# Optimization experiments

Hardware: AMD Instinct MI355X
Metric: run time of the kernel (lower is better)

## Reference

```python
import jax, jax.numpy as jnp
import numpy as np

EPS = 1e-5  # BatchNorm eps (eval mode, running mean 0 / var 1)
NEG_SLOPE = 0.2


def _knn_idx(x, k):
    # x: [B,C,N] -> idx [B,N,k] (indices of k largest of negative sq dist = k nearest)
    inner = jnp.einsum('bcn,bcm->bnm', x, x)
    xx = jnp.sum(x * x, axis=1)  # [B,N]
    pd = 2.0 * inner - xx[:, :, None] - xx[:, None, :]
    return jax.lax.top_k(pd, k)[1]


def _edge_feature(x, k):
    # x: [B,C,N] -> edge features [B,2C,N,k] = concat(neighbor - center, center)
    idx = _knn_idx(x, k)                        # [B,N,k]
    xt = jnp.transpose(x, (0, 2, 1))            # [B,N,C]
    nbr = jax.vmap(lambda f, i: f[i])(xt, idx)  # [B,N,k,C] gather per batch
    ctr = jnp.broadcast_to(xt[:, :, None, :], nbr.shape)
    feat = jnp.concatenate([nbr - ctr, ctr], axis=-1)  # [B,N,k,2C]
    return jnp.transpose(feat, (0, 3, 1, 2))


def _bn(x, g, b):
    # eval-mode BatchNorm: running_mean=0, running_var=1 -> x * g/sqrt(1+eps) + b
    inv = 1.0 / np.sqrt(1.0 + EPS)
    sh = (1, -1) + (1,) * (x.ndim - 2)
    return x * (g * inv).reshape(sh) + b.reshape(sh)


def _lrelu(x):
    return jnp.where(x >= 0, x, NEG_SLOPE * x)


def _conv2d(x, w, b):  # 1x1 Conv2d: x [B,Ci,N,K], w [Ci,Co]
    return jnp.einsum('bcnk,co->bonk', x, w) + b[None, :, None, None]


def _conv1d(x, w, b):  # 1x1 Conv1d: x [B,Ci,N], w [Ci,Co]
    return jnp.einsum('bcn,co->bon', x, w) + b[None, :, None]


def setup_inputs() -> dict:
    key = jax.random.key(0)
    ks = jax.random.split(key, 24)
    B, N = 8, 4096
    rn = lambda k, sh, s=0.1: (jax.random.normal(k, sh, dtype=jnp.float32) * s)
    inp = {
        'point': jax.random.normal(ks[0], (B, 3, N), dtype=jnp.float32),
        # conv1_1: Conv2d(6,64)
        'w11': rn(ks[1], (6, 64)), 'b11': rn(ks[2], (64,)),
        'g11': jnp.ones((64,), jnp.float32), 'bb11': jnp.zeros((64,), jnp.float32),
        # conv1_2: Conv2d(6,64)
        'w12': rn(ks[3], (6, 64)), 'b12': rn(ks[4], (64,)),
        'g12': jnp.ones((64,), jnp.float32), 'bb12': jnp.zeros((64,), jnp.float32),
        # conv1_3: Conv1d(128,64)
        'w13': rn(ks[5], (128, 64)), 'b13': rn(ks[6], (64,)),
        'g13': jnp.ones((64,), jnp.float32), 'bb13': jnp.zeros((64,), jnp.float32),
        # conv1_5: Conv2d(128,64)
        'w15': rn(ks[7], (128, 64)), 'b15': rn(ks[8], (64,)),
        'g15': jnp.ones((64,), jnp.float32), 'bb15': jnp.zeros((64,), jnp.float32),
        # conv1_4: Conv1d(64,128)
        'w14': rn(ks[9], (64, 128)), 'b14': rn(ks[10], (128,)),
        'g14': jnp.ones((128,), jnp.float32), 'bb14': jnp.zeros((128,), jnp.float32),
        # fc1: Linear(128,64) + ReLU + Linear(64,3)
        'wf1': rn(ks[11], (128, 64)), 'bf1': rn(ks[12], (64,)),
        'wf2': rn(ks[13], (64, 3)), 'bf2': rn(ks[14], (3,)),
    }
    return inp


def reference(point, w11, b11, g11, bb11, w12, b12, g12, bb12,
              w13, b13, g13, bb13, w15, b15, g15, bb15,
              w14, b14, g14, bb14, wf1, bf1, wf2, bf2):
    # point: [B,3,N]
    f = _edge_feature(point, 8)                    # [B,6,N,8]
    f1 = _lrelu(_bn(_conv2d(f, w11, b11), g11, bb11)).max(axis=-1)   # [B,64,N]
    f = _edge_feature(point, 16)                   # [B,6,N,16]
    f2 = _lrelu(_bn(_conv2d(f, w12, b12), g12, bb12)).max(axis=-1)   # [B,64,N]
    f = jnp.concatenate([f1, f2], axis=1)          # [B,128,N]
    f = _lrelu(_bn(_conv1d(f, w13, b13), g13, bb13))                 # [B,64,N]
    g = _edge_feature(f, 16)                       # [B,128,N,16]
    g = _lrelu(_bn(_conv2d(g, w15, b15), g15, bb15)).max(axis=-1)    # [B,64,N]
    g = _lrelu(_bn(_conv1d(g, w14, b14), g14, bb14))                 # [B,128,N]
    feat = jnp.transpose(g, (0, 2, 1))             # [B,N,128]
    h = jax.nn.relu(feat @ wf1 + bf1) @ wf2 + bf2  # [B,N,3]
    refinepoint = h + jnp.transpose(point, (0, 2, 1))
    return feat, refinepoint
```

## Files before the change

kernel.cpp:

```cpp
#include <hip/hip_runtime.h>
#include <math.h>

#define NB 8
#define NP 4096
#define FEAT_SZ (NB * NP * 128)
#define INVBN 0.9999950000374999f
#define SPLIT 2
#define CHUNKS 32

typedef unsigned long long u64;
typedef unsigned int u32;

__device__ __forceinline__ u32 fmap(float f) {
    u32 b = __float_as_uint(f);
    return b ^ ((u32)((int)b >> 31) | 0x80000000u);
}

__device__ __forceinline__ u64 umax64(u64 a, u64 b) { return a > b ? a : b; }

__device__ __forceinline__ void kins(u64 (&v)[16], u64 key) {
    if (key <= v[15]) return;
    bool bb[16];
#pragma unroll
    for (int j = 0; j < 16; ++j) bb[j] = key > v[j];
#pragma unroll
    for (int j = 15; j >= 1; --j) v[j] = bb[j] ? (bb[j - 1] ? v[j - 1] : key) : v[j];
    if (bb[0]) v[0] = key;
}

__device__ __forceinline__ void bufpush(u64 (&v)[16], u64 &q0, u64 &q1, u64 &q2, u64 &q3,
                                        int &cnt, u64 key) {
    if (cnt < 4) {
        q0 = cnt == 0 ? key : q0;
        q1 = cnt == 1 ? key : q1;
        q2 = cnt == 2 ? key : q2;
        q3 = cnt == 3 ? key : q3;
        ++cnt;
    } else {
        kins(v, key);
    }
}

__device__ __forceinline__ void bufflush(u64 (&v)[16], u64 &q0, u64 &q1, u64 &q2, u64 &q3,
                                         int &cnt) {
    kins(v, q0); kins(v, q1); kins(v, q2); kins(v, q3);
    q0 = 0; q1 = 0; q2 = 0; q3 = 0; cnt = 0;
}

__device__ __forceinline__ void bclean(u64 (&v)[16]) {
#pragma unroll
    for (int d = 8; d; d >>= 1) {
#pragma unroll
        for (int i = 0; i < 16; ++i) {
            if ((i & d) == 0) {
                u64 a = v[i], b = v[i | d];
                bool s = a < b;
                v[i] = s ? b : a;
                v[i | d] = s ? a : b;
            }
        }
    }
}

__device__ __forceinline__ void merge_shfl(u64 (&v)[16], int off) {
    u64 o[16];
#pragma unroll
    for (int j = 0; j < 16; ++j) o[j] = __shfl_down(v[j], off);
#pragma unroll
    for (int j = 0; j < 16; ++j) {
        u64 b = o[15 - j];
        v[j] = v[j] > b ? v[j] : b;
    }
    bclean(v);
}

__device__ __forceinline__ u64 rowmax8(u64 x) {
    x = umax64(x, __shfl_xor(x, 1));
    x = umax64(x, __shfl_xor(x, 2));
    x = umax64(x, __shfl_xor(x, 4));
    return x;
}

__global__ __launch_bounds__(256) void knn_point_kernel(const float* __restrict__ point,
                                                        int* __restrict__ idxP) {
    __shared__ float4 pts[NP];
    int bt = blockIdx.x >> 7;
    int n0 = (blockIdx.x & 127) << 5;
    const float* pb = point + (size_t)bt * 3 * NP;
    for (int m = threadIdx.x; m < NP; m += 256) {
        float x = pb[m], y = pb[NP + m], z = pb[2 * NP + m];
        pts[m] = make_float4(x, y, z, fmaf(z, z, fmaf(y, y, x * x)));
    }
    __syncthreads();
    int t = threadIdx.x;
    int q = t & 7;
    float4 c = pts[n0 + (t >> 3)];
    u64 v[16];
#pragma unroll
    for (int j = 0; j < 16; ++j) v[j] = 0;
    u64 b0 = 0, b1 = 0, b2 = 0, b3 = 0;
    int cnt = 0;
    u64 th = 0;
#pragma unroll 1
    for (int o = 0; o < 8; ++o) {
#pragma unroll 4
        for (int ii = 0; ii < 64; ++ii) {
            int m = (((o << 6) + ii) << 3) + q;
            float4 p = pts[m];
            float inner = fmaf(c.z, p.z, fmaf(c.y, p.y, c.x * p.x));
            float pd = fmaf(2.0f, inner, -c.w) - p.w;
            u64 key = ((u64)fmap(pd) << 32) | (u64)(u32)~m;
            if (key > th) bufpush(v, b0, b1, b2, b3, cnt, key);
        }
        if (__any(cnt >= 3)) {
            bufflush(v, b0, b1, b2, b3, cnt);
            th = rowmax8(v[15]);
        }
    }
    bufflush(v, b0, b1, b2, b3, cnt);
    merge_shfl(v, 4);
    merge_shfl(v, 2);
    merge_shfl(v, 1);
    if (q == 0) {
        int* op = idxP + ((size_t)bt * NP + n0 + (t >> 3)) * 16;
#pragma unroll
        for (int j = 0; j < 16; ++j) op[j] = (int)~(u32)v[j];
    }
}

__global__ __launch_bounds__(256) void edge12_kernel(
    const float* __restrict__ point, const int* __restrict__ idxP,
    const float* __restrict__ w11, const float* __restrict__ b11,
    const float* __restrict__ g11, const float* __restrict__ bb11,
    const float* __restrict__ w12, const float* __restrict__ b12,
    const float* __restrict__ g12, const float* __restrict__ bb12,
    float* __restrict__ f12) {
    int lane = threadIdx.x & 63;
    int pt = blockIdx.x * 4 + (threadIdx.x >> 6);
    int bt = pt >> 12, n = pt & (NP - 1);
    const float* pb = point + (size_t)bt * 3 * NP;
    float wd1[3], wc1[3], wd2[3], wc2[3];
#pragma unroll
    for (int c = 0; c < 3; ++c) {
        wd1[c] = w11[c * 64 + lane]; wc1[c] = w11[(3 + c) * 64 + lane];
        wd2[c] = w12[c * 64 + lane]; wc2[c] = w12[(3 + c) * 64 + lane];
    }
    float s1 = g11[lane] * INVBN, sh1 = bb11[lane];
    float s2 = g12[lane] * INVBN, sh2 = bb12[lane];
    float cx = pb[n], cy = pb[NP + n], cz = pb[2 * NP + n];
    float base1 = fmaf(wc1[2], cz, fmaf(wc1[1], cy, fmaf(wc1[0], cx, b11[lane])));
    float base2 = fmaf(wc2[2], cz, fmaf(wc2[1], cy, fmaf(wc2[0], cx, b12[lane])));
    float a1 = -INFINITY, a2 = -INFINITY;
    const int* nb = idxP + (size_t)pt * 16;
#pragma unroll
    for (int j = 0; j < 16; ++j) {
        int m = nb[j];
        float ex = pb[m] - cx, ey = pb[NP + m] - cy, ez = pb[2 * NP + m] - cz;
        float y2 = fmaf(wd2[2], ez, fmaf(wd2[1], ey, fmaf(wd2[0], ex, base2)));
        float z2 = fmaf(y2, s2, sh2);
        z2 = z2 >= 0.f ? z2 : 0.2f * z2;
        a2 = fmaxf(a2, z2);
        if (j < 8) {
            float y1 = fmaf(wd1[2], ez, fmaf(wd1[1], ey, fmaf(wd1[0], ex, base1)));
            float z1 = fmaf(y1, s1, sh1);
            z1 = z1 >= 0.f ? z1 : 0.2f * z1;
            a1 = fmaxf(a1, z1);
        }
    }
    f12[((size_t)pt << 7) + lane] = a1;
    f12[((size_t)pt << 7) + 64 + lane] = a2;
}

template<int K, int O, int MODE, bool XX>
__global__ __launch_bounds__(256) void gemm_act_kernel(
        const float* __restrict__ in, const float* __restrict__ W,
        const float* __restrict__ b, const float* __restrict__ g,
        const float* __restrict__ s, float* __restrict__ outp,
        float* __restrict__ xxo) {
    __shared__ __align__(16) char smem[64 * (K + 1) * 4 + K * O * 4];
    float* A  = (float*)smem;
    float* Wl = (float*)(smem + 64 * (K + 1) * 4);
    float* Hs = (float*)smem;
    constexpr int F4R = K / 4;
#pragma unroll
    for (int i = 0; i < 64 * F4R / 256; ++i) {
        int f = threadIdx.x + i * 256;
        int pt = f / F4R, c4 = f % F4R;
        float4 v = *(const float4*)(in + ((size_t)blockIdx.x * 64 + pt) * K + c4 * 4);
        float* d = A + pt * (K + 1) + c4 * 4;
        d[0] = v.x; d[1] = v.y; d[2] = v.z; d[3] = v.w;
    }
    if constexpr (MODE == 0) {
#pragma unroll
        for (int i = 0; i < 8; ++i) {
            int f = threadIdx.x + i * 256;
            int half = f >= 1024;
            int fr = f & 1023;
            int c = fr >> 4, o4 = fr & 15;
            const float* src = half ? (W + (64 + c) * 64 + o4 * 4) : (W + c * 64 + o4 * 4);
            float4 v = *(const float4*)src;
            float* d = Wl + c * 128 + half * 64 + o4 * 4;
            d[0] = v.x; d[1] = v.y; d[2] = v.z; d[3] = v.w;
        }
    } else {
#pragma unroll
        for (int i = 0; i < K * O / 1024; ++i) {
            int f = threadIdx.x + i * 256;
            *(float4*)(Wl + f * 4) = *(const float4*)(W + f * 4);
        }
    }
    __syncthreads();
    constexpr int NO = O / 8;
    int po = threadIdx.x & 7, pp = threadIdx.x >> 3;
    int pt0 = pp * 2, o0 = po * NO;
    float acc[2][NO];
#pragma unroll
    for (int i = 0; i < NO; ++i) {
        int o = o0 + i;
        float init;
        if constexpr (MODE == 0) init = (o < 64) ? 0.f : b[o - 64];
        else init = b[o];
        acc[0][i] = init;
        acc[1][i] = init;
    }
#pragma unroll 8
    for (int kk = 0; kk < K; ++kk) {
        float a0 = A[pt0 * (K + 1) + kk];
        float a1 = A[(pt0 + 1) * (K + 1) + kk];
        float w[NO];
#pragma unroll
        for (int i4 = 0; i4 < NO / 4; ++i4) {
            float4 wv = *(const float4*)(Wl + kk * O + o0 + i4 * 4);
            w[i4 * 4 + 0] = wv.x; w[i4 * 4 + 1] = wv.y;
            w[i4 * 4 + 2] = wv.z; w[i4 * 4 + 3] = wv.w;
        }
#pragma unroll
        for (int i = 0; i < NO; ++i) {
            acc[0][i] = fmaf(a0, w[i], acc[0][i]);
            acc[1][i] = fmaf(a1, w[i], acc[1][i]);
        }
    }
    float tact[2][NO];
#pragma unroll
    for (int p = 0; p < 2; ++p) {
#pragma unroll
        for (int i = 0; i < NO; ++i) {
            int o = o0 + i;
            float a = acc[p][i];
            if constexpr (MODE == 0) {
                tact[p][i] = a;
            } else {
                float vv = fmaf(a, g[o] * INVBN, s[o]);
                tact[p][i] = vv >= 0.f ? vv : 0.2f * vv;
            }
        }
    }
#pragma unroll
    for (int p = 0; p < 2; ++p) {
        size_t rowg = (size_t)blockIdx.x * 64 + pt0 + p;
#pragma unroll
        for (int i4 = 0; i4 < NO / 4; ++i4) {
            float4 ov;
            ov.x = tact[p][i4 * 4 + 0]; ov.y = tact[p][i4 * 4 + 1];
            ov.z = tact[p][i4 * 4 + 2]; ov.w = tact[p][i4 * 4 + 3];
            *(float4*)(outp + rowg * O + o0 + i4 * 4) = ov;
        }
    }
    if constexpr (XX) {
        __syncthreads();
#pragma unroll
        for (int p = 0; p < 2; ++p)
#pragma unroll
            for (int i = 0; i < NO; ++i)
                Hs[(pt0 + p) * 65 + o0 + i] = tact[p][i];
        __syncthreads();
        if (threadIdx.x < 64) {
            float ss = 0.f;
#pragma unroll
            for (int c = 0; c < 64; ++c) {
                float hc = Hs[threadIdx.x * 65 + c];
                ss = fmaf(hc, hc, ss);
            }
            xxo[(size_t)blockIdx.x * 64 + threadIdx.x] = ss;
        }
    }
}

__global__ __launch_bounds__(256, 2) void knn_feat_kernel(const float* __restrict__ h1t,
                                                          const float* __restrict__ xxf,
                                                          u64* __restrict__ partF) {
    __shared__ __align__(16) char smem[81920];
    float* At = (float*)smem;
    float* Bt = (float*)(smem + 32768);
    u32*   Sb = (u32*)(smem + 49152);
    int seg = blockIdx.x & 1;
    int rg  = (blockIdx.x >> 1) & 31;
    int bt  = blockIdx.x >> 6;
    int n0  = rg << 7;
    int tid = threadIdx.x;
    int rp = tid >> 4;
    int cg = tid & 15;
    int cs = cg << 2;
    const float* hbase = h1t + ((size_t)bt * NP << 6);
    const float* hA = hbase + ((size_t)n0 << 6);
#pragma unroll
    for (int rep = 0; rep < 8; ++rep) {
        int row = rep * 16 + rp;
        float4 va = *(const float4*)(hA + (row << 6) + cs);
        float fv[4] = {va.x, va.y, va.z, va.w};
#pragma unroll
        for (int i = 0; i < 4; ++i) {
            int ch = cs + i;
            int rw = row ^ ((row & 32) >> 3) ^ (((ch >> 2) & 7) << 2);
            At[ch * 128 + rw] = fv[i];
        }
    }
    int m00 = seg * (CHUNKS * 64);
#pragma unroll
    for (int rep = 0; rep < 4; ++rep) {
        int col = rep * 16 + rp;
        float4 vb = *(const float4*)(hbase + ((size_t)(m00 + col) << 6) + cs);
        float fv[4] = {vb.x, vb.y, vb.z, vb.w};
#pragma unroll
        for (int i = 0; i < 4; ++i) {
            int ch = cs + i;
            int cl = col ^ ((col & 32) >> 3) ^ (((ch >> 2) & 7) << 2);
            Bt[ch * 64 + cl] = fv[i];
        }
    }
    float xa[8];
    {
        const float* xap = xxf + bt * NP + n0 + rp * 8;
        float4 t0 = *(const float4*)xap;
        float4 t1 = *(const float4*)(xap + 4);
        xa[0]=t0.x; xa[1]=t0.y; xa[2]=t0.z; xa[3]=t0.w;
        xa[4]=t1.x; xa[5]=t1.y; xa[6]=t1.z; xa[7]=t1.w;
    }
    int r = tid >> 1, h = tid & 1;
    u64 v[16];
#pragma unroll
    for (int j = 0; j < 16; ++j) v[j] = 0;
    u64 q0 = 0, q1 = 0, q2 = 0, q3 = 0;
    int cnt = 0;
    u32 th32 = 0;
    int ab0 = (rp * 8) ^ (rp & 4);
    int ab1 = (rp * 8 + 4) ^ (rp & 4);
    int cb0 = (cg * 4) ^ ((cg & 8) >> 1);
    int swQ = ((r ^ (r >> 3)) & 7) << 2;
    __syncthreads();
#pragma unroll 1
    for (int mcl = 0; mcl < CHUNKS; ++mcl) {
        int m0c = m00 + (mcl << 6);
        bool more = (mcl + 1) < CHUNKS;
        float4 nv0, nv1, nv2, nv3;
        if (more) {
            const float* hn = hbase + ((size_t)(m0c + 64) << 6);
            nv0 = *(const float4*)(hn + ((0 * 16 + rp) << 6) + cs);
            nv1 = *(const float4*)(hn + ((1 * 16 + rp) << 6) + cs);
            nv2 = *(const float4*)(hn + ((2 * 16 + rp) << 6) + cs);
            nv3 = *(const float4*)(hn + ((3 * 16 + rp) << 6) + cs);
        }
        float4 xbv = *(const float4*)(xxf + bt * NP + m0c + (cg << 2));
        float acc[8][4];
#pragma unroll
        for (int i = 0; i < 8; ++i)
#pragma unroll
            for (int j = 0; j < 4; ++j) acc[i][j] = 0.f;
#pragma unroll 1
        for (int gI = 0; gI < 16; ++gI) {
            int sw = (gI & 7) << 2;
            const float* pa0 = At + (gI << 9) + (ab0 ^ sw);
            const float* pa1 = At + (gI << 9) + (ab1 ^ sw);
            const float* pbq = Bt + (gI << 8) + (cb0 ^ sw);
#pragma unroll
            for (int u = 0; u < 4; ++u) {
                float4 a0 = *(const float4*)(pa0 + (u << 7));
                float4 a1 = *(const float4*)(pa1 + (u << 7));
                float4 bq = *(const float4*)(pbq + (u << 6));
                float av[8] = {a0.x, a0.y, a0.z, a0.w, a1.x, a1.y, a1.z, a1.w};
                float bv[4] = {bq.x, bq.y, bq.z, bq.w};
#pragma unroll
                for (int i = 0; i < 8; ++i)
#pragma unroll
                    for (int j = 0; j < 4; ++j)
                        acc[i][j] = fmaf(av[i], bv[j], acc[i][j]);
            }
        }
        float xbs[4] = {xbv.x, xbv.y, xbv.z, xbv.w};
#pragma unroll
        for (int i = 0; i < 8; ++i) {
            int row = rp * 8 + i;
            u32 k0, k1, k2, k3;
            {
                float pd;
                pd = fmaf(2.0f, acc[i][0], -xa[i]) - xbs[0]; k0 = fmap(pd);
                pd = fmaf(2.0f, acc[i][1], -xa[i]) - xbs[1]; k1 = fmap(pd);
                pd = fmaf(2.0f, acc[i][2], -xa[i]) - xbs[2]; k2 = fmap(pd);
                pd = fmaf(2.0f, acc[i][3], -xa[i]) - xbs[3]; k3 = fmap(pd);
            }
            int sq = ((row ^ (row >> 3)) & 7) << 2;
            *(uint4*)(Sb + row * 64 + ((cg << 2) ^ sq)) = make_uint4(k0, k1, k2, k3);
        }
        __syncthreads();
#pragma unroll
        for (int sI = 0; sI < 8; ++sI) {
            int c0 = h * 32 + (sI << 2);
            uint4 kq = *(const uint4*)(Sb + r * 64 + (c0 ^ swQ));
            u32 m01 = kq.x > kq.y ? kq.x : kq.y;
            u32 m23 = kq.z > kq.w ? kq.z : kq.w;
            u32 mx = m01 > m23 ? m01 : m23;
            if (mx >= th32) {
                u32 ks[4] = {kq.x, kq.y, kq.z, kq.w};
#pragma unroll
                for (int j = 0; j < 4; ++j) {
                    if (ks[j] >= th32) {
                        u64 key = ((u64)ks[j] << 32) | (u64)(u32)~(m0c + c0 + j);
                        bufpush(v, q0, q1, q2, q3, cnt, key);
                    }
                }
            }
        }
        if (more) {
            float fva[4][4] = {{nv0.x, nv0.y, nv0.z, nv0.w}, {nv1.x, nv1.y, nv1.z, nv1.w},
                               {nv2.x, nv2.y, nv2.z, nv2.w}, {nv3.x, nv3.y, nv3.z, nv3.w}};
#pragma unroll
            for (int rep = 0; rep < 4; ++rep) {
                int col = rep * 16 + rp;
#pragma unroll
                for (int i = 0; i < 4; ++i) {
                    int ch = cs + i;
                    int cl = col ^ ((col & 32) >> 3) ^ (((ch >> 2) & 7) << 2);
                    Bt[ch * 64 + cl] = fva[rep][i];
                }
            }
        }
        if (__any(cnt >= 3)) {
            bufflush(v, q0, q1, q2, q3, cnt);
            u64 m = umax64(v[15], __shfl_xor(v[15], 1));
            th32 = (u32)(m >> 32);
        }
        __syncthreads();
    }
    bufflush(v, q0, q1, q2, q3, cnt);
    merge_shfl(v, 1);
    if (h == 0) {
        u64* op = partF + (((size_t)bt * NP + n0 + r) * SPLIT + seg) * 16;
#pragma unroll
        for (int j = 0; j < 16; ++j) op[j] = v[j];
    }
}

__global__ __launch_bounds__(256, 3) void edge5_gemm14_kernel(
        const float* __restrict__ ZC, const u64* __restrict__ partF,
        const float* __restrict__ g15, const float* __restrict__ bb15,
        const float* __restrict__ w14, const float* __restrict__ b14,
        const float* __restrict__ g14, const float* __restrict__ bb14,
        float* __restrict__ feat) {
    __shared__ int midx[64][16];
    __shared__ float Ag[64 * 65];
    __shared__ float Wl[64 * 128];
    int tid = threadIdx.x;
#pragma unroll
    for (int i = 0; i < 8; ++i) {
        int f = tid + i * 256;
        *(float4*)(Wl + f * 4) = *(const float4*)(w14 + f * 4);
    }
    if (tid < 64) {
        int pt = blockIdx.x * 64 + tid;
        const u64* base = partF + (size_t)pt * (SPLIT * 16);
        u64 a[16];
#pragma unroll
        for (int j = 0; j < 16; ++j) a[j] = base[j];
#pragma unroll
        for (int j = 0; j < 16; ++j) {
            u64 x = base[16 + (15 - j)];
            a[j] = a[j] > x ? a[j] : x;
        }
        bclean(a);
#pragma unroll
        for (int j = 0; j < 16; ++j) midx[tid][j] = (int)~(u32)a[j];
    }
    __syncthreads();
    int lane = tid & 63, w = tid >> 6;
    int bt = (blockIdx.x * 64) >> 12;
    const float* zb = ZC + (((size_t)bt * NP) << 7);
    float sc = g15[lane] * INVBN, sh = bb15[lane];
#pragma unroll 1
    for (int pp = 0; pp < 16; ++pp) {
        int p = w * 16 + pp;
        int pt = blockIdx.x * 64 + p;
        const float* zrow = ZC + ((size_t)pt << 7);
        float zn = zrow[lane];
        float d = zrow[64 + lane] - zn;
        float zl[16];
#pragma unroll
        for (int j = 0; j < 16; ++j)
            zl[j] = zb[((size_t)midx[p][j] << 7) + lane];
        float a = -INFINITY;
#pragma unroll
        for (int j = 0; j < 16; ++j) {
            float z = fmaf(zl[j] + d, sc, sh);
            z = z >= 0.f ? z : 0.2f * z;
            a = fmaxf(a, z);
        }
        Ag[p * 65 + lane] = a;
    }
    __syncthreads();
    int po = tid & 7, pq = tid >> 3;
    int pt0 = pq * 2, o0 = po * 16;
    float acc[2][16];
#pragma unroll
    for (int i = 0; i < 16; ++i) { acc[0][i] = b14[o0 + i]; acc[1][i] = b14[o0 + i]; }
#pragma unroll 8
    for (int kk = 0; kk < 64; ++kk) {
        float a0 = Ag[pt0 * 65 + kk];
        float a1 = Ag[(pt0 + 1) * 65 + kk];
        float wv[16];
#pragma unroll
        for (int i4 = 0; i4 < 4; ++i4) {
            float4 t = *(const float4*)(Wl + kk * 128 + o0 + i4 * 4);
            wv[i4 * 4 + 0] = t.x; wv[i4 * 4 + 1] = t.y;
            wv[i4 * 4 + 2] = t.z; wv[i4 * 4 + 3] = t.w;
        }
#pragma unroll
        for (int i = 0; i < 16; ++i) {
            acc[0][i] = fmaf(a0, wv[i], acc[0][i]);
            acc[1][i] = fmaf(a1, wv[i], acc[1][i]);
        }
    }
#pragma unroll
    for (int p = 0; p < 2; ++p) {
        size_t rowg = (size_t)blockIdx.x * 64 + pt0 + p;
#pragma unroll
        for (int i4 = 0; i4 < 4; ++i4) {
            float4 ov;
#pragma unroll
            for (int j = 0; j < 4; ++j) {
                int o = o0 + i4 * 4 + j;
                float vv = fmaf(acc[p][i4 * 4 + j], g14[o] * INVBN, bb14[o]);
                ((float*)&ov)[j] = vv >= 0.f ? vv : 0.2f * vv;
            }
            *(float4*)(feat + rowg * 128 + o0 + i4 * 4) = ov;
        }
    }
}

__global__ __launch_bounds__(256) void fc_head_kernel(const float* __restrict__ feat,
        const float* __restrict__ point,
        const float* __restrict__ wf1, const float* __restrict__ bf1,
        const float* __restrict__ wf2, const float* __restrict__ bf2,
        float* __restrict__ out) {
    __shared__ float A[64 * 129];
    __shared__ float Wl[128 * 64];
    __shared__ float wf2l[192];
    float* R = Wl;
#pragma unroll
    for (int i = 0; i < 8; ++i) {
        int f = threadIdx.x + i * 256;
        int pt = f >> 5, c4 = f & 31;
        float4 v = *(const float4*)(feat + ((size_t)blockIdx.x * 64 + pt) * 128 + c4 * 4);
        float* d = A + pt * 129 + c4 * 4;
        d[0] = v.x; d[1] = v.y; d[2] = v.z; d[3] = v.w;
    }
#pragma unroll
    for (int i = 0; i < 8; ++i) {
        int f = threadIdx.x + i * 256;
        *(float4*)(Wl + f * 4) = *(const float4*)(wf1 + f * 4);
    }
    if (threadIdx.x < 48)
        *(float4*)(wf2l + threadIdx.x * 4) = *(const float4*)(wf2 + threadIdx.x * 4);
    __syncthreads();
    int po = threadIdx.x & 7, pp = threadIdx.x >> 3;
    int pt0 = pp * 2, o0 = po * 8;
    float acc[2][8];
#pragma unroll
    for (int i = 0; i < 8; ++i) { acc[0][i] = bf1[o0 + i]; acc[1][i] = bf1[o0 + i]; }
#pragma unroll 8
    for (int kk = 0; kk < 128; ++kk) {
        float a0 = A[pt0 * 129 + kk];
        float a1 = A[(pt0 + 1) * 129 + kk];
        float w[8];
#pragma unroll
        for (int i4 = 0; i4 < 2; ++i4) {
            float4 wv = *(const float4*)(Wl + kk * 64 + o0 + i4 * 4);
            w[i4 * 4 + 0] = wv.x; w[i4 * 4 + 1] = wv.y;
            w[i4 * 4 + 2] = wv.z; w[i4 * 4 + 3] = wv.w;
        }
#pragma unroll
        for (int i = 0; i < 8; ++i) {
            acc[0][i] = fmaf(a0, w[i], acc[0][i]);
            acc[1][i] = fmaf(a1, w[i], acc[1][i]);
        }
    }
    __syncthreads();
#pragma unroll
    for (int p = 0; p < 2; ++p)
#pragma unroll
        for (int i = 0; i < 8; ++i)
            R[(pt0 + p) * 65 + o0 + i] = fmaxf(acc[p][i], 0.f);
    __syncthreads();
    if (threadIdx.x < 192) {
        int pt = threadIdx.x / 3, dim = threadIdx.x - pt * 3;
        float ssum = 0.f;
#pragma unroll
        for (int c = 0; c < 64; ++c)
            ssum = fmaf(R[pt * 65 + c], wf2l[c * 3 + dim], ssum);
        int ptg = blockIdx.x * 64 + pt;
        int bt = ptg >> 12, n = ptg & (NP - 1);
        float p = point[((size_t)bt * 3 + dim) * NP + n];
        out[(size_t)FEAT_SZ + (size_t)ptg * 3 + dim] = ssum + bf2[dim] + p;
    }
}

extern "C" void kernel_launch(void* const* d_in, const int* in_sizes, int n_in,
                              void* d_out, int out_size, void* d_ws, size_t ws_size,
                              hipStream_t stream) {
    (void)in_sizes; (void)n_in; (void)out_size; (void)ws_size;
    const float* point = (const float*)d_in[0];
    const float* w11 = (const float*)d_in[1];
    const float* b11 = (const float*)d_in[2];
    const float* g11 = (const float*)d_in[3];
    const float* bb11 = (const float*)d_in[4];
    const float* w12 = (const float*)d_in[5];
    const float* b12 = (const float*)d_in[6];
    const float* g12 = (const float*)d_in[7];
    const float* bb12 = (const float*)d_in[8];
    const float* w13 = (const float*)d_in[9];
    const float* b13 = (const float*)d_in[10];
    const float* g13 = (const float*)d_in[11];
    const float* bb13 = (const float*)d_in[12];
    const float* w15 = (const float*)d_in[13];
    const float* b15 = (const float*)d_in[14];
    const float* g15 = (const float*)d_in[15];
    const float* bb15 = (const float*)d_in[16];
    const float* w14 = (const float*)d_in[17];
    const float* b14 = (const float*)d_in[18];
    const float* g14 = (const float*)d_in[19];
    const float* bb14 = (const float*)d_in[20];
    const float* wf1 = (const float*)d_in[21];
    const float* bf1 = (const float*)d_in[22];
    const float* wf2 = (const float*)d_in[23];
    const float* bf2 = (const float*)d_in[24];

    char* ws = (char*)d_ws;
    int*   idxP  = (int*)ws;
    float* xxf   = (float*)(ws + (2u << 20));
    float* h1t   = (float*)(ws + (4u << 20));
    u64*   partF = (u64*)(ws + (12u << 20));
    float* f12   = (float*)(ws + (20u << 20));
    float* ZC    = (float*)(ws + (20u << 20));
    float* feat  = (float*)d_out;

    knn_point_kernel<<<dim3(NB * 128), dim3(256), 0, stream>>>(point, idxP);
    edge12_kernel<<<dim3(NB * NP / 4), dim3(256), 0, stream>>>(
        point, idxP, w11, b11, g11, bb11, w12, b12, g12, bb12, f12);
    gemm_act_kernel<128, 64, 1, true><<<dim3(NB * NP / 64), dim3(256), 0, stream>>>(
        f12, w13, b13, g13, bb13, h1t, xxf);
    knn_feat_kernel<<<dim3(NB * 32 * SPLIT), dim3(256), 0, stream>>>(h1t, xxf, partF);
    gemm_act_kernel<64, 128, 0, false><<<dim3(NB * NP / 64), dim3(256), 0, stream>>>(
        h1t, w15, b15, nullptr, nullptr, ZC, nullptr);
    edge5_gemm14_kernel<<<dim3(NB * NP / 64), dim3(256), 0, stream>>>(
        ZC, partF, g15, bb15, w14, b14, g14, bb14, feat);
    fc_head_kernel<<<dim3(NB * NP / 64), dim3(256), 0, stream>>>(
        feat, point, wf1, bf1, wf2, bf2, (float*)d_out);
}
```

Before: 945.6 us.

## Fuse point kNN with edge12 conv and process two queries per thread

Merges the point-cloud kNN kernel with the edge-feature conv kernel, so neighbour indices stay in shared memory and neighbour coordinates are read from the already-staged LDS point array. This removes the idxP global round trip and one launch. It also changes the kNN split from 8 lanes per query to 16 lanes handling two queries each, so every shared-memory point load is reused for two distance computations. In exchange, register pressure roughly doubles from the two top-16 lists and their buffers, and the merge needs an extra shuffle stage.

```diff
diff --git a/kernel.cpp b/kernel.cpp
--- a/kernel.cpp
+++ b/kernel.cpp
@@ -74,16 +74,23 @@
     bclean(v);
 }
 
-__device__ __forceinline__ u64 rowmax8(u64 x) {
+__device__ __forceinline__ u64 rowmax16(u64 x) {
     x = umax64(x, __shfl_xor(x, 1));
     x = umax64(x, __shfl_xor(x, 2));
     x = umax64(x, __shfl_xor(x, 4));
+    x = umax64(x, __shfl_xor(x, 8));
     return x;
 }
 
-__global__ __launch_bounds__(256) void knn_point_kernel(const float* __restrict__ point,
-                                                        int* __restrict__ idxP) {
+__global__ __launch_bounds__(256) void knn_point_edge12_kernel(
+    const float* __restrict__ point,
+    const float* __restrict__ w11, const float* __restrict__ b11,
+    const float* __restrict__ g11, const float* __restrict__ bb11,
+    const float* __restrict__ w12, const float* __restrict__ b12,
+    const float* __restrict__ g12, const float* __restrict__ bb12,
+    float* __restrict__ f12) {
     __shared__ float4 pts[NP];
+    __shared__ int midx[32][16];
     int bt = blockIdx.x >> 7;
     int n0 = (blockIdx.x & 127) << 5;
     const float* pb = point + (size_t)bt * 3 * NP;
@@ -93,52 +100,52 @@
     }
     __syncthreads();
     int t = threadIdx.x;
-    int q = t & 7;
-    float4 c = pts[n0 + (t >> 3)];
-    u64 v[16];
-#pragma unroll
-    for (int j = 0; j < 16; ++j) v[j] = 0;
-    u64 b0 = 0, b1 = 0, b2 = 0, b3 = 0;
-    int cnt = 0;
-    u64 th = 0;
+    int q = t & 15;
+    int rq = t >> 4;
+    float4 c0 = pts[n0 + rq * 2];
+    float4 c1 = pts[n0 + rq * 2 + 1];
+    u64 v0[16], v1[16];
+#pragma unroll
+    for (int j = 0; j < 16; ++j) { v0[j] = 0; v1[j] = 0; }
+    u64 A0 = 0, A1 = 0, A2 = 0, A3 = 0;
+    u64 B0 = 0, B1 = 0, B2 = 0, B3 = 0;
+    int cA = 0, cB = 0;
+    u64 th0 = 0, th1 = 0;
 #pragma unroll 1
     for (int o = 0; o < 8; ++o) {
 #pragma unroll 4
-        for (int ii = 0; ii < 64; ++ii) {
-            int m = (((o << 6) + ii) << 3) + q;
+        for (int ii = 0; ii < 32; ++ii) {
+            int m = (((o << 5) + ii) << 4) + q;
             float4 p = pts[m];
-            float inner = fmaf(c.z, p.z, fmaf(c.y, p.y, c.x * p.x));
-            float pd = fmaf(2.0f, inner, -c.w) - p.w;
-            u64 key = ((u64)fmap(pd) << 32) | (u64)(u32)~m;
-            if (key > th) bufpush(v, b0, b1, b2, b3, cnt, key);
-        }
-        if (__any(cnt >= 3)) {
-            bufflush(v, b0, b1, b2, b3, cnt);
-            th = rowmax8(v[15]);
-        }
-    }
-    bufflush(v, b0, b1, b2, b3, cnt);
-    merge_shfl(v, 4);
-    merge_shfl(v, 2);
-    merge_shfl(v, 1);
+            float in0 = fmaf(c0.z, p.z, fmaf(c0.y, p.y, c0.x * p.x));
+            float pd0 = fmaf(2.0f, in0, -c0.w) - p.w;
+            u64 k0 = ((u64)fmap(pd0) << 32) | (u64)(u32)~m;
+            if (k0 > th0) bufpush(v0, A0, A1, A2, A3, cA, k0);
+            float in1 = fmaf(c1.z, p.z, fmaf(c1.y, p.y, c1.x * p.x));
+            float pd1 = fmaf(2.0f, in1, -c1.w) - p.w;
+            u64 k1 = ((u64)fmap(pd1) << 32) | (u64)(u32)~m;
+            if (k1 > th1) bufpush(v1, B0, B1, B2, B3, cB, k1);
+        }
+        if (__any((cA >= 3) || (cB >= 3))) {
+            bufflush(v0, A0, A1, A2, A3, cA);
+            bufflush(v1, B0, B1, B2, B3, cB);
+            th0 = rowmax16(v0[15]);
+            th1 = rowmax16(v1[15]);
+        }
+    }
+    bufflush(v0, A0, A1, A2, A3, cA);
+    bufflush(v1, B0, B1, B2, B3, cB);
+    merge_shfl(v0, 8); merge_shfl(v0, 4); merge_shfl(v0, 2); merge_shfl(v0, 1);
+    merge_shfl(v1, 8); merge_shfl(v1, 4); merge_shfl(v1, 2); merge_shfl(v1, 1);
     if (q == 0) {
-        int* op = idxP + ((size_t)bt * NP + n0 + (t >> 3)) * 16;
-#pragma unroll
-        for (int j = 0; j < 16; ++j) op[j] = (int)~(u32)v[j];
-    }
-}
-
-__global__ __launch_bounds__(256) void edge12_kernel(
-    const float* __restrict__ point, const int* __restrict__ idxP,
-    const float* __restrict__ w11, const float* __restrict__ b11,
-    const float* __restrict__ g11, const float* __restrict__ bb11,
-    const float* __restrict__ w12, const float* __restrict__ b12,
-    const float* __restrict__ g12, const float* __restrict__ bb12,
-    float* __restrict__ f12) {
-    int lane = threadIdx.x & 63;
-    int pt = blockIdx.x * 4 + (threadIdx.x >> 6);
-    int bt = pt >> 12, n = pt & (NP - 1);
-    const float* pb = point + (size_t)bt * 3 * NP;
+#pragma unroll
+        for (int j = 0; j < 16; ++j) {
+            midx[rq * 2][j] = (int)~(u32)v0[j];
+            midx[rq * 2 + 1][j] = (int)~(u32)v1[j];
+        }
+    }
+    __syncthreads();
+    int lane = t & 63, w = t >> 6;
     float wd1[3], wc1[3], wd2[3], wc2[3];
 #pragma unroll
     for (int c = 0; c < 3; ++c) {
@@ -147,28 +154,33 @@
     }
     float s1 = g11[lane] * INVBN, sh1 = bb11[lane];
     float s2 = g12[lane] * INVBN, sh2 = bb12[lane];
-    float cx = pb[n], cy = pb[NP + n], cz = pb[2 * NP + n];
-    float base1 = fmaf(wc1[2], cz, fmaf(wc1[1], cy, fmaf(wc1[0], cx, b11[lane])));
-    float base2 = fmaf(wc2[2], cz, fmaf(wc2[1], cy, fmaf(wc2[0], cx, b12[lane])));
-    float a1 = -INFINITY, a2 = -INFINITY;
-    const int* nb = idxP + (size_t)pt * 16;
-#pragma unroll
-    for (int j = 0; j < 16; ++j) {
-        int m = nb[j];
-        float ex = pb[m] - cx, ey = pb[NP + m] - cy, ez = pb[2 * NP + m] - cz;
-        float y2 = fmaf(wd2[2], ez, fmaf(wd2[1], ey, fmaf(wd2[0], ex, base2)));
-        float z2 = fmaf(y2, s2, sh2);
-        z2 = z2 >= 0.f ? z2 : 0.2f * z2;
-        a2 = fmaxf(a2, z2);
-        if (j < 8) {
-            float y1 = fmaf(wd1[2], ez, fmaf(wd1[1], ey, fmaf(wd1[0], ex, base1)));
-            float z1 = fmaf(y1, s1, sh1);
-            z1 = z1 >= 0.f ? z1 : 0.2f * z1;
-            a1 = fmaxf(a1, z1);
-        }
-    }
-    f12[((size_t)pt << 7) + lane] = a1;
-    f12[((size_t)pt << 7) + 64 + lane] = a2;
+#pragma unroll 1
+    for (int pp = 0; pp < 8; ++pp) {
+        int pl = w * 8 + pp;
+        size_t pt = (size_t)bt * NP + n0 + pl;
+        float4 cc = pts[n0 + pl];
+        float base1 = fmaf(wc1[2], cc.z, fmaf(wc1[1], cc.y, fmaf(wc1[0], cc.x, b11[lane])));
+        float base2 = fmaf(wc2[2], cc.z, fmaf(wc2[1], cc.y, fmaf(wc2[0], cc.x, b12[lane])));
+        float a1 = -INFINITY, a2 = -INFINITY;
+#pragma unroll
+        for (int j = 0; j < 16; ++j) {
+            int m = midx[pl][j];
+            float4 pm = pts[m];
+            float ex = pm.x - cc.x, ey = pm.y - cc.y, ez = pm.z - cc.z;
+            float y2 = fmaf(wd2[2], ez, fmaf(wd2[1], ey, fmaf(wd2[0], ex, base2)));
+            float z2 = fmaf(y2, s2, sh2);
+            z2 = z2 >= 0.f ? z2 : 0.2f * z2;
+            a2 = fmaxf(a2, z2);
+            if (j < 8) {
+                float y1 = fmaf(wd1[2], ez, fmaf(wd1[1], ey, fmaf(wd1[0], ex, base1)));
+                float z1 = fmaf(y1, s1, sh1);
+                z1 = z1 >= 0.f ? z1 : 0.2f * z1;
+                a1 = fmaxf(a1, z1);
+            }
+        }
+        f12[(pt << 7) + lane] = a1;
+        f12[(pt << 7) + 64 + lane] = a2;
+    }
 }
 
 template<int K, int O, int MODE, bool XX>
@@ -643,7 +655,6 @@
     const float* bf2 = (const float*)d_in[24];
 
     char* ws = (char*)d_ws;
-    int*   idxP  = (int*)ws;
     float* xxf   = (float*)(ws + (2u << 20));
     float* h1t   = (float*)(ws + (4u << 20));
     u64*   partF = (u64*)(ws + (12u << 20));
@@ -651,9 +662,8 @@
     float* ZC    = (float*)(ws + (20u << 20));
     float* feat  = (float*)d_out;
 
-    knn_point_kernel<<<dim3(NB * 128), dim3(256), 0, stream>>>(point, idxP);
-    edge12_kernel<<<dim3(NB * NP / 4), dim3(256), 0, stream>>>(
-        point, idxP, w11, b11, g11, bb11, w12, b12, g12, bb12, f12);
+    knn_point_edge12_kernel<<<dim3(NB * 128), dim3(256), 0, stream>>>(
+        point, w11, b11, g11, bb11, w12, b12, g12, bb12, f12);
     gemm_act_kernel<128, 64, 1, true><<<dim3(NB * NP / 64), dim3(256), 0, stream>>>(
         f12, w13, b13, g13, bb13, h1t, xxf);
     knn_feat_kernel<<<dim3(NB * 32 * SPLIT), dim3(256), 0, stream>>>(h1t, xxf, partF);
```

After: 965.0 us. 2.1% more time.
